# Kernel tuning notes

Hardware: AMD Instinct MI355X
Metric: run time of the kernel (lower is better)

Reference implementation:

```python
import jax, jax.numpy as jnp
import numpy as np

D_MODEL = 1024
NUM_HEADS = 16
D_K = D_MODEL // NUM_HEADS


def setup_inputs() -> dict:
    key = jax.random.key(0)
    ks = jax.random.split(key, 11)
    B, S = 4, 2048
    s = 1.0 / np.sqrt(D_MODEL)
    inp = {
        'q': jax.random.normal(ks[0], (B, S, D_MODEL), dtype=jnp.float32),
        'k': jax.random.normal(ks[1], (B, S, D_MODEL), dtype=jnp.float32),
        'v': jax.random.normal(ks[2], (B, S, D_MODEL), dtype=jnp.float32),
        'Wq': jax.random.normal(ks[3], (D_MODEL, D_MODEL), dtype=jnp.float32) * s,
        'bq': jnp.zeros((D_MODEL,), dtype=jnp.float32),
        'Wk': jax.random.normal(ks[4], (D_MODEL, D_MODEL), dtype=jnp.float32) * s,
        'bk': jnp.zeros((D_MODEL,), dtype=jnp.float32),
        'Wv': jax.random.normal(ks[5], (D_MODEL, D_MODEL), dtype=jnp.float32) * s,
        'bv': jnp.zeros((D_MODEL,), dtype=jnp.float32),
        'Wo': jax.random.normal(ks[6], (D_MODEL, D_MODEL), dtype=jnp.float32) * s,
        'bo': jnp.zeros((D_MODEL,), dtype=jnp.float32),
    }
    return inp


def _split_heads(x):
    B, S, _ = x.shape
    return x.reshape(B, S, NUM_HEADS, D_K).transpose(0, 2, 1, 3)  # [B,H,S,d_k]


def reference(q, k, v, Wq, bq, Wk, bk, Wv, bv, Wo, bo):
    B, S, _ = q.shape
    qh = _split_heads(q @ Wq.T + bq)
    kh = _split_heads(k @ Wk.T + bk)
    vh = _split_heads(v @ Wv.T + bv)
    scale = 1.0 / jnp.sqrt(jnp.asarray(D_K, dtype=qh.dtype))
    scores = jnp.einsum('bhqd,bhkd->bhqk', qh, kh) * scale  # [B,H,S,S]
    attn = jax.nn.softmax(scores, axis=-1)
    out = jnp.einsum('bhqk,bhkd->bhqd', attn, vh)  # [B,H,S,d_k]
    out = out.transpose(0, 2, 1, 3).reshape(B, S, D_MODEL)
    return out @ Wo.T + bo
```

## Files before the change

### kernel.cpp

```cpp
#include <hip/hip_runtime.h>


typedef __bf16 bf16_t;
typedef bf16_t bf16x8 __attribute__((ext_vector_type(8)));
typedef bf16_t bf16x4 __attribute__((ext_vector_type(4)));
typedef float  f32x4  __attribute__((ext_vector_type(4)));
typedef short  s16x4  __attribute__((ext_vector_type(4)));

#define MFMA16(A, B, C) __builtin_amdgcn_mfma_f32_16x16x32_bf16(A, B, C, 0, 0, 0)

static __device__ __forceinline__ f32x4 mfma16k16(bf16x4 a, bf16x4 b, f32x4 c) {
  return __builtin_amdgcn_mfma_f32_16x16x16bf16_1k(
      __builtin_bit_cast(s16x4, a), __builtin_bit_cast(s16x4, b), c, 0, 0, 0);
}

#define NB   4
#define SEQ  2048
#define DM   1024
#define NH   16
#define DK   64
#define MTOT (NB * SEQ)
#define QSCALE 0.18033688011112042f

__device__ __forceinline__ void async_copy16(bf16_t* lds, const bf16_t* gsrc) {
  __builtin_amdgcn_global_load_lds(
      (const __attribute__((address_space(1))) unsigned int*)gsrc,
      (__attribute__((address_space(3))) unsigned int*)lds, 16, 0, 0);
}

__device__ __forceinline__ float fast_exp2(float x) {
#if __has_builtin(__builtin_amdgcn_exp2f)
  return __builtin_amdgcn_exp2f(x);
#else
  return exp2f(x);
#endif
}

__global__ __launch_bounds__(256) void cvt3(const float* __restrict__ a,
                                            const float* __restrict__ b,
                                            const float* __restrict__ c,
                                            bf16_t* __restrict__ oa,
                                            bf16_t* __restrict__ ob,
                                            bf16_t* __restrict__ oc, int n4) {
  const int z = blockIdx.y;
  const float* s = (z == 0) ? a : (z == 1) ? b : c;
  bf16_t* d = (z == 0) ? oa : (z == 1) ? ob : oc;
  int i = blockIdx.x * 256 + threadIdx.x;
  if (i < n4) {
    f32x4 v = ((const f32x4*)s)[i];
    ((bf16x4*)d)[i] = __builtin_convertvector(v, bf16x4);
  }
}

__global__ __launch_bounds__(256) void cvt4(const float* __restrict__ a,
                                            const float* __restrict__ b,
                                            const float* __restrict__ c,
                                            const float* __restrict__ dd,
                                            bf16_t* __restrict__ oa,
                                            bf16_t* __restrict__ ob,
                                            bf16_t* __restrict__ oc,
                                            bf16_t* __restrict__ od, int n4) {
  const int z = blockIdx.y;
  const float* s = (z == 0) ? a : (z == 1) ? b : (z == 2) ? c : dd;
  bf16_t* d = (z == 0) ? oa : (z == 1) ? ob : (z == 2) ? oc : od;
  int i = blockIdx.x * 256 + threadIdx.x;
  if (i < n4) {
    f32x4 v = ((const f32x4*)s)[i];
    ((bf16x4*)d)[i] = __builtin_convertvector(v, bf16x4);
  }
}

__device__ __forceinline__ void gemm_core_1024(const bf16_t* __restrict__ A,
                                               const bf16_t* __restrict__ W,
                                               bf16_t* sA, bf16_t* sB,
                                               f32x4 (&acc)[4][4], int m0, int n0) {
  const int tid = threadIdx.x;
  const int lane = tid & 63, r = lane & 15, qd = lane >> 4;
  const int wave = tid >> 6;
  const int wm = (wave & 1) * 64, wn = (wave >> 1) * 64;
  const int arow = tid >> 2, cc = tid & 3;
  const int achk = (cc ^ ((arow >> 1) & 3)) * 8;
  const bf16_t* gA = A + (size_t)(m0 + arow) * DM + achk;
  const bf16_t* gB = W + (size_t)(n0 + arow) * DM + achk;
  bf16_t* lA = sA + arow * 32 + cc * 8;
  bf16_t* lB = sB + arow * 32 + cc * 8;
  const int gsw = (qd ^ ((r >> 1) & 3)) * 8;

#define GSTAGE(buf, k0)                                                       \
  do {                                                                        \
    async_copy16(lA + (buf) * 4096,           gA + (k0));                     \
    async_copy16(lA + (buf) * 4096 + 64 * 32, gA + (k0) + (size_t)64 * DM);   \
    async_copy16(lB + (buf) * 4096,           gB + (k0));                     \
    async_copy16(lB + (buf) * 4096 + 64 * 32, gB + (k0) + (size_t)64 * DM);   \
  } while (0)

  GSTAGE(0, 0);
#pragma unroll 2
  for (int k0 = 0; k0 < DM; k0 += 32) {
    const int buf = (k0 >> 5) & 1;
    __syncthreads();
    if (k0 + 32 < DM) GSTAGE(buf ^ 1, k0 + 32);

    const bf16_t* cA = sA + buf * 4096;
    const bf16_t* cB = sB + buf * 4096;
    bf16x8 af[4], bw[4];
#pragma unroll
    for (int i = 0; i < 4; i++)
      af[i] = *(const bf16x8*)(cA + (wm + i * 16 + r) * 32 + gsw);
#pragma unroll
    for (int j = 0; j < 4; j++)
      bw[j] = *(const bf16x8*)(cB + (wn + j * 16 + r) * 32 + gsw);
#pragma unroll
    for (int i = 0; i < 4; i++)
#pragma unroll
      for (int j = 0; j < 4; j++)
        acc[i][j] = MFMA16(af[i], bw[j], acc[i][j]);
  }
#undef GSTAGE
}

__global__ __launch_bounds__(256)
void gemm_qkv(const bf16_t* __restrict__ qb, const bf16_t* __restrict__ kb,
              const bf16_t* __restrict__ vb, const bf16_t* __restrict__ wq,
              const bf16_t* __restrict__ wk, const bf16_t* __restrict__ wv,
              const float* __restrict__ bq, const float* __restrict__ bk,
              const float* __restrict__ bv, bf16_t* __restrict__ Qh,
              bf16_t* __restrict__ Kh, bf16_t* __restrict__ Vt) {
  __shared__ __align__(16) bf16_t sA[2 * 128 * 32];
  __shared__ __align__(16) bf16_t sB[2 * 128 * 32];
  const int z = blockIdx.z;
  const bf16_t* A = (z == 0) ? qb : (z == 1) ? kb : vb;
  const bf16_t* W = (z == 0) ? wq : (z == 1) ? wk : wv;
  const float* bias = (z == 0) ? bq : (z == 1) ? bk : bv;
  const int m0 = blockIdx.x * 128, n0 = blockIdx.y * 128;

  f32x4 acc[4][4] = {};
  gemm_core_1024(A, W, sA, sB, acc, m0, n0);

  const int tid = threadIdx.x, lane = tid & 63, r = lane & 15, qd = lane >> 4;
  const int wave = tid >> 6, wm = (wave & 1) * 64, wn = (wave >> 1) * 64;
#pragma unroll
  for (int j = 0; j < 4; j++) {
    const int n = n0 + wn + j * 16 + r;
    const float bs = bias[n];
    const int h = n >> 6, d = n & 63;
#pragma unroll
    for (int i = 0; i < 4; i++) {
#pragma unroll
      for (int rr = 0; rr < 4; rr++) {
        const int m = m0 + wm + i * 16 + qd * 4 + rr;
        const int b_ = m >> 11, s_ = m & 2047;
        float v = acc[i][j][rr] + bs;
        if (z == 0) {
          v *= QSCALE;
          Qh[(((size_t)b_ * NH + h) * SEQ + s_) * DK + d] = (bf16_t)v;
        } else if (z == 1) {
          Kh[(((size_t)b_ * NH + h) * SEQ + s_) * DK + d] = (bf16_t)v;
        } else {
          Vt[(((size_t)b_ * NH + h) * DK + d) * SEQ + (s_ ^ ((d & 1) * 4))] =
              (bf16_t)v;
        }
      }
    }
  }
}

__global__ __launch_bounds__(256)
void gemm_out(const bf16_t* __restrict__ A, const bf16_t* __restrict__ W,
              const float* __restrict__ bias, float* __restrict__ C) {
  __shared__ __align__(16) bf16_t sA[2 * 128 * 32];
  __shared__ __align__(16) bf16_t sB[2 * 128 * 32];
  const int m0 = blockIdx.x * 128, n0 = blockIdx.y * 128;
  f32x4 acc[4][4] = {};
  gemm_core_1024(A, W, sA, sB, acc, m0, n0);

  const int tid = threadIdx.x, lane = tid & 63, r = lane & 15, qd = lane >> 4;
  const int wave = tid >> 6, wm = (wave & 1) * 64, wn = (wave >> 1) * 64;
#pragma unroll
  for (int j = 0; j < 4; j++) {
    const int n = n0 + wn + j * 16 + r;
    const float bs = bias[n];
#pragma unroll
    for (int i = 0; i < 4; i++) {
#pragma unroll
      for (int rr = 0; rr < 4; rr++) {
        const int m = m0 + wm + i * 16 + qd * 4 + rr;
        C[(size_t)m * DM + n] = acc[i][j][rr] + bs;
      }
    }
  }
}

__global__ __launch_bounds__(256, 4)
void attn(const bf16_t* __restrict__ Qh, const bf16_t* __restrict__ Kh,
          const bf16_t* __restrict__ Vt, bf16_t* __restrict__ Ah) {
  __shared__ __align__(16) bf16_t sK[2][64 * 64];
  __shared__ __align__(16) bf16_t sV[2][64 * 64];

  const int tid = threadIdx.x, wave = tid >> 6, lane = tid & 63;
  const int r = lane & 15, qd = lane >> 4;
  const int id = blockIdx.x;
  const int xcd = id & 7, sub = id >> 3;
  const int bh = xcd * 8 + (sub >> 4);
  const int q0 = (sub & 15) * 128 + wave * 32;
  const size_t bK = (size_t)bh * SEQ * DK;
  const size_t bV = (size_t)bh * DK * SEQ;

  bf16x8 aq[2][2];
#pragma unroll
  for (int qt = 0; qt < 2; qt++)
#pragma unroll
    for (int hf = 0; hf < 2; hf++)
      aq[qt][hf] = *(const bf16x8*)(Qh + bK + (size_t)(q0 + qt * 16 + r) * DK +
                                    hf * 32 + qd * 8);

  f32x4 o[4][2] = {};
  f32x4 lacc[2] = {};
  bf16x4 vone;
#pragma unroll
  for (int i = 0; i < 4; i++) vone[i] = (bf16_t)1.0f;

  const int srow = tid >> 3, sc = tid & 7;
  const bf16_t* pK = Kh + bK + (size_t)srow * DK + ((sc ^ (srow & 7)) * 8);
  const bf16_t* pV = Vt + bV + (size_t)srow * SEQ + ((sc ^ ((srow >> 1) & 7)) * 8);

  const int kswz0 = (qd ^ (r & 7)) * 8;
  const int kswz1 = ((4 + qd) ^ (r & 7)) * 8;

#define STAGE(buf)                                                             \
  do {                                                                         \
    async_copy16(&sK[buf][0] + tid * 8,        pK);                            \
    async_copy16(&sK[buf][0] + 2048 + tid * 8, pK + (size_t)32 * DK);          \
    async_copy16(&sV[buf][0] + tid * 8,        pV);                            \
    async_copy16(&sV[buf][0] + 2048 + tid * 8, pV + (size_t)32 * SEQ);         \
    pK += (size_t)64 * DK;                                                     \
    pV += 64;                                                                  \
  } while (0)

#define QKT(buf, mt, par)                                                      \
  do {                                                                         \
    bf16x8 ka0 = *(const bf16x8*)(&sK[buf][0] + ((mt)*16 + r) * 64 + kswz0);   \
    bf16x8 ka1 = *(const bf16x8*)(&sK[buf][0] + ((mt)*16 + r) * 64 + kswz1);   \
    f32x4 z_ = {0.f, 0.f, 0.f, 0.f};                                           \
    s[par][0] = MFMA16(ka0, aq[0][0], z_);                                     \
    s[par][1] = MFMA16(ka0, aq[1][0], z_);                                     \
    s[par][0] = MFMA16(ka1, aq[0][1], s[par][0]);                              \
    s[par][1] = MFMA16(ka1, aq[1][1], s[par][1]);                              \
  } while (0)

#define EXPCVT(mt, par)                                                        \
  do {                                                                         \
    f32x4 e0_, e1_;                                                            \
    _Pragma("unroll") for (int rr = 0; rr < 4; rr++)                           \
        e0_[rr] = fast_exp2(s[par][0][rr]);                                    \
    _Pragma("unroll") for (int rr = 0; rr < 4; rr++)                           \
        e1_[rr] = fast_exp2(s[par][1][rr]);                                    \
    p[0][mt] = __builtin_convertvector(e0_, bf16x4);                           \
    p[1][mt] = __builtin_convertvector(e1_, bf16x4);                           \
  } while (0)

#define COMPUTE(buf)                                                           \
  do {                                                                         \
    f32x4 s[2][2];                            \
    bf16x4 p[2][4];                                              \
    QKT(buf, 0, 0);                                                            \
    QKT(buf, 1, 1);                                                            \
    EXPCVT(0, 0);                                                              \
    QKT(buf, 2, 0);                                                            \
    EXPCVT(1, 1);                                                              \
    QKT(buf, 3, 1);                                                            \
    EXPCVT(2, 0);                                                              \
    EXPCVT(3, 1);                                                              \
    _Pragma("unroll") for (int mt = 0; mt < 4; mt++) {                         \
      const bf16_t* vb_ = &sV[buf][0] + (((mt * 4 + qd) ^ r) * 4) + r * 64;    \
      bf16x4 va0 = *(const bf16x4*)(vb_);                                      \
      bf16x4 va1 = *(const bf16x4*)(vb_ + 16 * 64);                            \
      bf16x4 va2 = *(const bf16x4*)(vb_ + 32 * 64);                            \
      bf16x4 va3 = *(const bf16x4*)(vb_ + 48 * 64);                            \
      lacc[0] = mfma16k16(vone, p[0][mt], lacc[0]);                            \
      o[0][0] = mfma16k16(va0, p[0][mt], o[0][0]);                             \
      o[0][1] = mfma16k16(va0, p[1][mt], o[0][1]);                             \
      o[1][0] = mfma16k16(va1, p[0][mt], o[1][0]);                             \
      o[1][1] = mfma16k16(va1, p[1][mt], o[1][1]);                             \
      lacc[1] = mfma16k16(vone, p[1][mt], lacc[1]);                            \
      o[2][0] = mfma16k16(va2, p[0][mt], o[2][0]);                             \
      o[2][1] = mfma16k16(va2, p[1][mt], o[2][1]);                             \
      o[3][0] = mfma16k16(va3, p[0][mt], o[3][0]);                             \
      o[3][1] = mfma16k16(va3, p[1][mt], o[3][1]);                             \
    }                                                                          \
  } while (0)

  STAGE(0);

#pragma unroll 1
  for (int it2 = 0; it2 < 16; it2++) {
    __syncthreads();
    STAGE(1);
    __builtin_amdgcn_s_setprio(1);
    COMPUTE(0);
    __builtin_amdgcn_s_setprio(0);
    __syncthreads();
    if (it2 < 15) STAGE(0);
    __builtin_amdgcn_s_setprio(1);
    COMPUTE(1);
    __builtin_amdgcn_s_setprio(0);
  }
#undef QKT
#undef EXPCVT
#undef COMPUTE
#undef STAGE

  const float linv0 = 1.0f / lacc[0][0];
  const float linv1 = 1.0f / lacc[1][0];
  const int b_ = bh >> 4, h_ = bh & 15;
#pragma unroll
  for (int qt = 0; qt < 2; qt++) {
    const float linv = qt ? linv1 : linv0;
    const size_t rowbase = ((size_t)b_ * SEQ + q0 + qt * 16 + r) * DM + h_ * DK;
#pragma unroll
    for (int dt = 0; dt < 4; dt++) {
      f32x4 w = o[dt][qt] * linv;
      *(bf16x4*)(Ah + rowbase + dt * 16 + qd * 4) =
          __builtin_convertvector(w, bf16x4);
    }
  }
}

extern "C" void kernel_launch(void* const* d_in, const int* in_sizes, int n_in,
                              void* d_out, int out_size, void* d_ws,
                              size_t ws_size, hipStream_t stream) {
  const float* q  = (const float*)d_in[0];
  const float* k  = (const float*)d_in[1];
  const float* v  = (const float*)d_in[2];
  const float* Wq = (const float*)d_in[3];
  const float* bq = (const float*)d_in[4];
  const float* Wk = (const float*)d_in[5];
  const float* bk = (const float*)d_in[6];
  const float* Wv = (const float*)d_in[7];
  const float* bv = (const float*)d_in[8];
  const float* Wo = (const float*)d_in[9];
  const float* bo = (const float*)d_in[10];

  char* ws = (char*)d_ws;
  const size_t SZ_QKV = (size_t)MTOT * DM * 2;
  const size_t SZ_W   = (size_t)DM * DM * 2;
  bf16_t* qb  = (bf16_t*)(ws);
  bf16_t* kb_ = (bf16_t*)(ws + SZ_QKV);
  bf16_t* vb  = (bf16_t*)(ws + 2 * SZ_QKV);
  bf16_t* Wqb = (bf16_t*)(ws + 3 * SZ_QKV);
  bf16_t* Wkb = (bf16_t*)(ws + 3 * SZ_QKV + SZ_W);
  bf16_t* Wvb = (bf16_t*)(ws + 3 * SZ_QKV + 2 * SZ_W);
  bf16_t* Wob = (bf16_t*)(ws + 3 * SZ_QKV + 3 * SZ_W);
  bf16_t* Qh  = (bf16_t*)(ws + 3 * SZ_QKV + 4 * SZ_W);
  bf16_t* Kh  = (bf16_t*)(ws + 4 * SZ_QKV + 4 * SZ_W);
  bf16_t* Vt  = (bf16_t*)(ws + 5 * SZ_QKV + 4 * SZ_W);
  bf16_t* Ah  = (bf16_t*)(ws + 6 * SZ_QKV + 4 * SZ_W);

  const int n4_qkv = MTOT * DM / 4;
  const int n4_w   = DM * DM / 4;
  cvt3<<<dim3(n4_qkv / 256, 3), 256, 0, stream>>>(q, k, v, qb, kb_, vb, n4_qkv);
  cvt4<<<dim3(n4_w / 256, 4), 256, 0, stream>>>(Wq, Wk, Wv, Wo, Wqb, Wkb, Wvb,
                                                Wob, n4_w);

  gemm_qkv<<<dim3(64, 8, 3), 256, 0, stream>>>(qb, kb_, vb, Wqb, Wkb, Wvb, bq,
                                               bk, bv, Qh, Kh, Vt);

  attn<<<dim3(1024), 256, 0, stream>>>(Qh, Kh, Vt, Ah);

  gemm_out<<<dim3(64, 8), 256, 0, stream>>>(Ah, Wob, bo, (float*)d_out);
}
```

Before: 366.4 us.

## Deepen GEMM LDS pipeline to four stages with explicit vmcnt waits

Replaces the double-buffered k-loop in the shared GEMM core with a four-buffer ring that keeps three tile loads in flight, using partial s_waitcnt vmcnt waits plus a raw barrier instead of __syncthreads. The goal is to hide global-load latency behind more MFMA work in both the QKV and output projections. LDS per block doubles to 64 KB, which may limit occupancy, and the hand-coded vmcnt counts depend on async_copy16 issuing exactly one memory op per call.

New measurement: 357.0 us. -2.6%, faster.

```diff
diff --git a/kernel.cpp b/kernel.cpp
--- a/kernel.cpp
+++ b/kernel.cpp
@@ -86,37 +86,55 @@
   bf16_t* lB = sB + arow * 32 + cc * 8;
   const int gsw = (qd ^ ((r >> 1) & 3)) * 8;
 
-#define GSTAGE(buf, k0)                                                       \
+#define GSTAGE4(buf)                                                          \
   do {                                                                        \
-    async_copy16(lA + (buf) * 4096,           gA + (k0));                     \
-    async_copy16(lA + (buf) * 4096 + 64 * 32, gA + (k0) + (size_t)64 * DM);   \
-    async_copy16(lB + (buf) * 4096,           gB + (k0));                     \
-    async_copy16(lB + (buf) * 4096 + 64 * 32, gB + (k0) + (size_t)64 * DM);   \
-  } while (0)
-
-  GSTAGE(0, 0);
-#pragma unroll 2
-  for (int k0 = 0; k0 < DM; k0 += 32) {
-    const int buf = (k0 >> 5) & 1;
-    __syncthreads();
-    if (k0 + 32 < DM) GSTAGE(buf ^ 1, k0 + 32);
-
-    const bf16_t* cA = sA + buf * 4096;
-    const bf16_t* cB = sB + buf * 4096;
-    bf16x8 af[4], bw[4];
-#pragma unroll
-    for (int i = 0; i < 4; i++)
-      af[i] = *(const bf16x8*)(cA + (wm + i * 16 + r) * 32 + gsw);
-#pragma unroll
-    for (int j = 0; j < 4; j++)
-      bw[j] = *(const bf16x8*)(cB + (wn + j * 16 + r) * 32 + gsw);
-#pragma unroll
-    for (int i = 0; i < 4; i++)
-#pragma unroll
-      for (int j = 0; j < 4; j++)
-        acc[i][j] = MFMA16(af[i], bw[j], acc[i][j]);
-  }
-#undef GSTAGE
+    async_copy16(lA + (buf) * 4096,           gA);                            \
+    async_copy16(lA + (buf) * 4096 + 64 * 32, gA + (size_t)64 * DM);          \
+    async_copy16(lB + (buf) * 4096,           gB);                            \
+    async_copy16(lB + (buf) * 4096 + 64 * 32, gB + (size_t)64 * DM);          \
+    gA += 32;                                                                 \
+    gB += 32;                                                                 \
+  } while (0)
+
+#define COMPUTE4(buf)                                                         \
+  do {                                                                        \
+    const bf16_t* cA = sA + (buf) * 4096;                                     \
+    const bf16_t* cB = sB + (buf) * 4096;                                     \
+    bf16x8 af[4], bw[4];                                                      \
+    _Pragma("unroll") for (int i_ = 0; i_ < 4; i_++)                          \
+        af[i_] = *(const bf16x8*)(cA + (wm + i_ * 16 + r) * 32 + gsw);        \
+    _Pragma("unroll") for (int j_ = 0; j_ < 4; j_++)                          \
+        bw[j_] = *(const bf16x8*)(cB + (wn + j_ * 16 + r) * 32 + gsw);        \
+    _Pragma("unroll") for (int i_ = 0; i_ < 4; i_++)                          \
+        _Pragma("unroll") for (int j_ = 0; j_ < 4; j_++)                      \
+            acc[i_][j_] = MFMA16(af[i_], bw[j_], acc[i_][j_]);                \
+  } while (0)
+
+#define WAITBAR(n)                                                            \
+  do {                                                                        \
+    asm volatile("s_waitcnt vmcnt(" #n ")" ::: "memory");                     \
+    __builtin_amdgcn_s_barrier();                                             \
+  } while (0)
+
+  GSTAGE4(0);
+  GSTAGE4(1);
+  GSTAGE4(2);
+
+#pragma unroll 1
+  for (int outer = 0; outer < 7; outer++) {
+    WAITBAR(8); GSTAGE4(3); COMPUTE4(0);
+    WAITBAR(8); GSTAGE4(0); COMPUTE4(1);
+    WAITBAR(8); GSTAGE4(1); COMPUTE4(2);
+    WAITBAR(8); GSTAGE4(2); COMPUTE4(3);
+  }
+  WAITBAR(8); GSTAGE4(3); COMPUTE4(0);
+  WAITBAR(8); COMPUTE4(1);
+  WAITBAR(4); COMPUTE4(2);
+  WAITBAR(0); COMPUTE4(3);
+
+#undef GSTAGE4
+#undef COMPUTE4
+#undef WAITBAR
 }
 
 __global__ __launch_bounds__(256)
@@ -126,8 +144,8 @@
               const float* __restrict__ bq, const float* __restrict__ bk,
               const float* __restrict__ bv, bf16_t* __restrict__ Qh,
               bf16_t* __restrict__ Kh, bf16_t* __restrict__ Vt) {
-  __shared__ __align__(16) bf16_t sA[2 * 128 * 32];
-  __shared__ __align__(16) bf16_t sB[2 * 128 * 32];
+  __shared__ __align__(16) bf16_t sA[4 * 128 * 32];
+  __shared__ __align__(16) bf16_t sB[4 * 128 * 32];
   const int z = blockIdx.z;
   const bf16_t* A = (z == 0) ? qb : (z == 1) ? kb : vb;
   const bf16_t* W = (z == 0) ? wq : (z == 1) ? wk : wv;
@@ -168,8 +186,8 @@
 __global__ __launch_bounds__(256)
 void gemm_out(const bf16_t* __restrict__ A, const bf16_t* __restrict__ W,
               const float* __restrict__ bias, float* __restrict__ C) {
-  __shared__ __align__(16) bf16_t sA[2 * 128 * 32];
-  __shared__ __align__(16) bf16_t sB[2 * 128 * 32];
+  __shared__ __align__(16) bf16_t sA[4 * 128 * 32];
+  __shared__ __align__(16) bf16_t sB[4 * 128 * 32];
   const int m0 = blockIdx.x * 128, n0 = blockIdx.y * 128;
   f32x4 acc[4][4] = {};
   gemm_core_1024(A, W, sA, sB, acc, m0, n0);
```
